# Kernel optimization log

Measured on AMD Instinct MI355X. Metric: run time of the kernel, lower is better.

The kernel has to match this reference:

```python
import jax, jax.numpy as jnp
import numpy as np

B, S, I, H = 32, 1024, 256, 256
NUM_LAYERS = 2


def _lstm_dir(x, m, h0, c0, Wih, Whh, bih, bhh, reverse=False):
    """x: [S,B,in], m: [S,B,1]. Returns outs [S,B,H], hT, cT.
    PyTorch LSTMCell gate order: i, f, g, o. Masked reset to init state per step."""
    if reverse:
        x = x[::-1]
        m = m[::-1]

    def step(carry, xm):
        h, c = carry
        xt, mt = xm
        gates = xt @ Wih.T + bih + h @ Whh.T + bhh  # [B,4H]
        i, f, g, o = jnp.split(gates, 4, axis=-1)
        i = jax.nn.sigmoid(i)
        f = jax.nn.sigmoid(f)
        g = jnp.tanh(g)
        o = jax.nn.sigmoid(o)
        cn = f * c + i * g
        hn = o * jnp.tanh(cn)
        hn = hn * mt + h0 * (1.0 - mt)
        cn = cn * mt + c0 * (1.0 - mt)
        return (hn, cn), hn

    (hT, cT), outs = jax.lax.scan(step, (h0, c0), (x, m))
    if reverse:
        outs = outs[::-1]
    return outs, hT, cT


def setup_inputs() -> dict:
    key = jax.random.key(0)
    ks = iter(jax.random.split(key, 40))
    d = {
        "inputs": jax.random.normal(next(ks), (B, S, I), dtype=jnp.float32),
        "mask": jnp.ones((B, S), dtype=jnp.float32),
    }
    scale = 0.05
    for li in range(NUM_LAYERS):
        in_sz = I if li == 0 else 2 * H
        for d_tag in ("f", "b"):
            p = f"l{li}{d_tag}_"
            d[p + "Wih"] = jax.random.normal(next(ks), (4 * H, in_sz), dtype=jnp.float32) * scale
            d[p + "Whh"] = jax.random.normal(next(ks), (4 * H, H), dtype=jnp.float32) * scale
            d[p + "bih"] = jnp.zeros((4 * H,), dtype=jnp.float32)
            d[p + "bhh"] = jnp.zeros((4 * H,), dtype=jnp.float32)
    return d


def reference(inputs, mask,
              l0f_Wih, l0f_Whh, l0f_bih, l0f_bhh,
              l0b_Wih, l0b_Whh, l0b_bih, l0b_bhh,
              l1f_Wih, l1f_Whh, l1f_bih, l1f_bhh,
              l1b_Wih, l1b_Whh, l1b_bih, l1b_bhh):
    # batch_first -> time-major
    x = jnp.transpose(inputs, (1, 0, 2))          # [S,B,I]
    m = jnp.transpose(mask, (1, 0))[:, :, None]   # [S,B,1] broadcasts over H
    h0 = jnp.zeros((B, H), dtype=inputs.dtype)
    c0 = h0

    layers = [
        ((l0f_Wih, l0f_Whh, l0f_bih, l0f_bhh), (l0b_Wih, l0b_Whh, l0b_bih, l0b_bhh)),
        ((l1f_Wih, l1f_Whh, l1f_bih, l1f_bhh), (l1b_Wih, l1b_Whh, l1b_bih, l1b_bhh)),
    ]
    hn, cn = [], []
    for fw_p, bw_p in layers:
        # (dropout between layers only active in training mode; eval reference skips it)
        fw_out, fh, fc = _lstm_dir(x, m, h0, c0, *fw_p, reverse=False)
        bw_out, bh, bc = _lstm_dir(x, m, h0, c0, *bw_p, reverse=True)
        x = jnp.concatenate((fw_out, bw_out), axis=2)  # [S,B,2H]
        hn.append(jnp.concatenate((fh, bh), axis=1))
        cn.append(jnp.concatenate((fc, bc), axis=1))

    output = jnp.transpose(x, (1, 0, 2))  # [B,S,2H]
    return output, jnp.stack(hn, axis=0), jnp.stack(cn, axis=0)
```

## Files before the change

### kernel.cpp

```cpp
#include <hip/hip_runtime.h>
#include <cstddef>

typedef __attribute__((ext_vector_type(8))) short short8;
typedef __attribute__((ext_vector_type(4))) short short4v;
typedef __attribute__((ext_vector_type(4))) float f32x4;

__device__ __forceinline__ unsigned short f2bf(float f){
  unsigned u = __builtin_bit_cast(unsigned, f);
  u += 0x7FFFu + ((u >> 16) & 1u);
  return (unsigned short)(u >> 16);
}
__device__ __forceinline__ float bf2f(unsigned short h){
  unsigned u = ((unsigned)h) << 16;
  return __builtin_bit_cast(float, u);
}
__device__ __forceinline__ float sigf(float x){
  return __builtin_amdgcn_rcpf(1.0f + __builtin_amdgcn_exp2f(-1.4426950408889634f * x));
}
__device__ __forceinline__ float tanhf_(float x){
  return 1.0f - 2.0f * __builtin_amdgcn_rcpf(1.0f + __builtin_amdgcn_exp2f(2.8853900817779268f * x));
}

__global__ __launch_bounds__(64) void cast_x(const float* __restrict__ in, unsigned short* __restrict__ xb){
  int blk = blockIdx.x;
  int t = blk & 1023, b = blk >> 10;
  int k = threadIdx.x * 4;
  float4 v = *(const float4*)(in + (size_t)blk * 256 + k);
  unsigned lo = f2bf(v.x) | ((unsigned)f2bf(v.y) << 16);
  unsigned hi = f2bf(v.z) | ((unsigned)f2bf(v.w) << 16);
  *(uint2*)(xb + ((size_t)t * 32 + b) * 256 + k) = make_uint2(lo, hi);
}

__global__ __launch_bounds__(64) void cast_w(const float* __restrict__ Wf, const float* __restrict__ Wb,
    const float* __restrict__ bihf, const float* __restrict__ bhhf,
    const float* __restrict__ bihb, const float* __restrict__ bhhb,
    unsigned short* __restrict__ Bw, float* __restrict__ bias, int K){
  int row = blockIdx.x;
  int dd = row >> 10, gc = row & 1023;
  const float* src = (dd ? Wb : Wf) + (size_t)gc * K;
  unsigned short* dst = Bw + (size_t)row * K;
  for (int k = threadIdx.x * 4; k < K; k += 256){
    float4 v = *(const float4*)(src + k);
    unsigned lo = f2bf(v.x) | ((unsigned)f2bf(v.y) << 16);
    unsigned hi = f2bf(v.z) | ((unsigned)f2bf(v.w) << 16);
    *(uint2*)(dst + k) = make_uint2(lo, hi);
  }
  if (threadIdx.x == 0)
    bias[row] = dd ? (bihb[gc] + bhhb[gc]) : (bihf[gc] + bhhf[gc]);
}

__global__ __launch_bounds__(256) void gemm_xg(const unsigned short* __restrict__ A,
    const unsigned short* __restrict__ Bw, const float* __restrict__ bias,
    unsigned short* __restrict__ xg, int K){
  __shared__ __align__(16) unsigned short Al[128 * 64];
  __shared__ __align__(16) unsigned short Bl[128 * 64];
  const int tid = threadIdx.x;
  const int w = tid >> 6, l = tid & 63, q = l >> 4, cl = l & 15;
  const int bm = blockIdx.x >> 4, bn = blockIdx.x & 15;
  const int wm = w & 1, wn = w >> 1;
  f32x4 acc[4][4];
#pragma unroll
  for (int nt = 0; nt < 4; ++nt){
    float bv = bias[bn * 128 + wn * 64 + nt * 16 + cl];
#pragma unroll
    for (int mt = 0; mt < 4; ++mt) acc[mt][nt] = (f32x4){bv, bv, bv, bv};
  }
  const unsigned short* Ab = A + (size_t)(bm * 128) * K;
  const unsigned short* Bb = Bw + (size_t)(bn * 128) * K;
  for (int k0 = 0; k0 < K; k0 += 64){
#pragma unroll
    for (int i = 0; i < 4; ++i){
      int task = tid + i * 256;
      int row = task >> 3, ch = task & 7;
      int sw = ((ch ^ (row & 7)) * 8);
      *(uint4*)(&Al[row * 64 + sw]) = *(const uint4*)(Ab + (size_t)row * K + k0 + ch * 8);
      *(uint4*)(&Bl[row * 64 + sw]) = *(const uint4*)(Bb + (size_t)row * K + k0 + ch * 8);
    }
    __syncthreads();
#pragma unroll
    for (int kt2 = 0; kt2 < 2; ++kt2){
      short8 af[4], bfv[4];
#pragma unroll
      for (int mt = 0; mt < 4; ++mt){
        int row = wm * 64 + mt * 16 + cl;
        af[mt] = *(const short8*)(&Al[row * 64 + (((kt2 * 4 + q) ^ (row & 7)) * 8)]);
      }
#pragma unroll
      for (int nt = 0; nt < 4; ++nt){
        int n = wn * 64 + nt * 16 + cl;
        bfv[nt] = *(const short8*)(&Bl[n * 64 + (((kt2 * 4 + q) ^ (n & 7)) * 8)]);
      }
#pragma unroll
      for (int mt = 0; mt < 4; ++mt)
#pragma unroll
        for (int nt = 0; nt < 4; ++nt)
          acc[mt][nt] = __builtin_amdgcn_mfma_f32_16x16x32_bf16(af[mt], bfv[nt], acc[mt][nt], 0, 0, 0);
    }
    __syncthreads();
  }
#pragma unroll
  for (int mt = 0; mt < 4; ++mt){
    int row = bm * 128 + wm * 64 + mt * 16 + q * 4;
    int tt = row >> 5, bb = row & 31;
#pragma unroll
    for (int nt = 0; nt < 4; ++nt){
      int col = bn * 128 + wn * 64 + nt * 16 + cl;
      f32x4 v = acc[mt][nt];
      unsigned lo = f2bf(v[0]) | ((unsigned)f2bf(v[1]) << 16);
      unsigned hi = f2bf(v[2]) | ((unsigned)f2bf(v[3]) << 16);
      *(uint2*)(xg + ((size_t)tt * 2048 + col) * 32 + bb) = make_uint2(lo, hi);
    }
  }
}

#define POLL1(EXTRA) \
  asm volatile("global_load_dwordx4 %0, %1, off sc1" EXTRA \
    : "=v"(pv) : "v"(pb) : "memory")

#define CHK() ( \
  xx = (pv.x ^ tagv) | (pv.y ^ tagv) | (pv.z ^ tagv) | (pv.w ^ tagv), \
  __all((xx & 0xFFFFu) == 0u) )

__global__ __launch_bounds__(512, 1) void lstm_rec(const unsigned short* __restrict__ xg,
    const float* __restrict__ WhhF, const float* __restrict__ WhhB,
    const float* __restrict__ mask, unsigned* __restrict__ hx,
    unsigned short* __restrict__ houts, float* __restrict__ out,
    float* __restrict__ hnout, float* __restrict__ cnout, int layer){
  __shared__ __align__(16) unsigned short hloc[2][16][136];
  __shared__ __align__(16) unsigned short hrem[2][16][136];
  __shared__ __align__(16) float maskL[16384];
  const int tid = threadIdx.x;
  const int w = tid >> 6, l = tid & 63, q = l >> 4, cl = l & 15;
  const int bid = blockIdx.x;
  const int ch = bid & 1, d = (bid >> 1) & 1, g = bid >> 2;
  const float* __restrict__ Whh = d ? WhhB : WhhF;
  const int jj = ch * 128 + w * 16 + cl;
  const int ph = ch ^ 1;
  const int ch4 = ch * 4, ph4 = ph * 4;

  short8 bfrag[4][8];
#pragma unroll
  for (int gi = 0; gi < 4; ++gi){
    const float* wg = Whh + (size_t)(gi * 256 + jj) * 256 + q * 8;
#pragma unroll
    for (int p = 0; p < 8; ++p){
      int gk = (p < 4) ? (ch4 + p) : (ph4 + (p - 4));
      float4 x0 = *(const float4*)(wg + gk * 32);
      float4 x1 = *(const float4*)(wg + gk * 32 + 4);
      short8 f;
      f[0] = (short)f2bf(x0.x); f[1] = (short)f2bf(x0.y); f[2] = (short)f2bf(x0.z); f[3] = (short)f2bf(x0.w);
      f[4] = (short)f2bf(x1.x); f[5] = (short)f2bf(x1.y); f[6] = (short)f2bf(x1.z); f[7] = (short)f2bf(x1.w);
      bfrag[gi][p] = f;
    }
  }
  for (int i = tid; i < 16384; i += 512){
    int tt = i >> 4, r = i & 15;
    maskL[i] = mask[(size_t)(g * 16 + r) * 1024 + tt];
  }
  __syncthreads();

  float cst[4] = {0.f, 0.f, 0.f, 0.f};
  unsigned* hxu = hx + (size_t)(d * 2 + g) * 8192;
  const int rr = 2 * w + (l >> 5);
  const int cc = l & 31;
  const unsigned* plA = hxu + rr * 256 + ph * 128 + cc * 4;
  const unsigned* plB = plA + 4096;
  unsigned* stA = hxu + (q * 4) * 256 + jj;
  unsigned* stB = stA + 4096;
  const int bq = g * 16 + q * 4;
  const size_t dj = (size_t)d * 256 + jj;
  unsigned short* hob = houts + (size_t)bq * 512 + dj;
  float* outb = out + (size_t)bq * 524288 + dj;

  const ptrdiff_t tstep = d ? -65536 : 65536;
  const unsigned short* xcur = xg + (size_t)(d ? 1023 : 0) * 65536
                               + ((size_t)d * 1024 + jj) * 32 + g * 16 + q * 4;
  short4v xp[4], xn[4];
#pragma unroll
  for (int gi = 0; gi < 4; ++gi) xp[gi] = *(const short4v*)(xcur + gi * 8192);

#pragma unroll 2
  for (int t = 0; t < 1024; ++t){
    const int par = t & 1;
    const int ot = d ? (1023 - t) : t;
    f32x4 acc[4];
    if (t > 0){
      const unsigned* pb = par ? plA : plB;
      uint4 pv;
      POLL1("");
#pragma unroll
      for (int gi = 0; gi < 4; ++gi)
        acc[gi] = (f32x4){bf2f((unsigned short)xp[gi][0]), bf2f((unsigned short)xp[gi][1]),
                          bf2f((unsigned short)xp[gi][2]), bf2f((unsigned short)xp[gi][3])};
      asm volatile("s_waitcnt vmcnt(0)" ::: "memory");
      __builtin_amdgcn_sched_barrier(0);
      const unsigned tagv = (unsigned)t;
      unsigned xx;
      if (!CHK()){
        do{
          POLL1("\n\ts_waitcnt vmcnt(0)");
          __builtin_amdgcn_sched_barrier(0);
        } while (!CHK());
      }
      if (t < 1023){
#pragma unroll
        for (int gi = 0; gi < 4; ++gi) xn[gi] = *(const short4v*)(xcur + tstep + gi * 8192);
      }
      {
        unsigned lo = __builtin_amdgcn_perm(pv.y, pv.x, 0x07060302u);
        unsigned hi = __builtin_amdgcn_perm(pv.w, pv.z, 0x07060302u);
        *(uint2*)(&hrem[par][rr][cc * 4]) = make_uint2(lo, hi);
      }
      __syncthreads();
      const unsigned short* lb = &hloc[par ^ 1][0][0];
      const unsigned short* rb = &hrem[par][0][0];
      const int ao = cl * 136 + q * 8;
#pragma unroll
      for (int ktl = 0; ktl < 4; ++ktl){
        short8 a = *(const short8*)(lb + ao + ktl * 32);
        acc[0] = __builtin_amdgcn_mfma_f32_16x16x32_bf16(a, bfrag[0][ktl], acc[0], 0, 0, 0);
        acc[1] = __builtin_amdgcn_mfma_f32_16x16x32_bf16(a, bfrag[1][ktl], acc[1], 0, 0, 0);
        acc[2] = __builtin_amdgcn_mfma_f32_16x16x32_bf16(a, bfrag[2][ktl], acc[2], 0, 0, 0);
        acc[3] = __builtin_amdgcn_mfma_f32_16x16x32_bf16(a, bfrag[3][ktl], acc[3], 0, 0, 0);
      }
#pragma unroll
      for (int ktl = 0; ktl < 4; ++ktl){
        short8 a = *(const short8*)(rb + ao + ktl * 32);
        acc[0] = __builtin_amdgcn_mfma_f32_16x16x32_bf16(a, bfrag[0][4 + ktl], acc[0], 0, 0, 0);
        acc[1] = __builtin_amdgcn_mfma_f32_16x16x32_bf16(a, bfrag[1][4 + ktl], acc[1], 0, 0, 0);
        acc[2] = __builtin_amdgcn_mfma_f32_16x16x32_bf16(a, bfrag[2][4 + ktl], acc[2], 0, 0, 0);
        acc[3] = __builtin_amdgcn_mfma_f32_16x16x32_bf16(a, bfrag[3][4 + ktl], acc[3], 0, 0, 0);
      }
    } else {
#pragma unroll
      for (int gi = 0; gi < 4; ++gi)
        acc[gi] = (f32x4){bf2f((unsigned short)xp[gi][0]), bf2f((unsigned short)xp[gi][1]),
                          bf2f((unsigned short)xp[gi][2]), bf2f((unsigned short)xp[gi][3])};
#pragma unroll
      for (int gi = 0; gi < 4; ++gi) xn[gi] = *(const short4v*)(xcur + tstep + gi * 8192);
    }
    f32x4 mv = *(const f32x4*)(&maskL[ot * 16 + q * 4]);
    float hv[4]; unsigned short hb[4];
#pragma unroll
    for (int r = 0; r < 4; ++r){
      float ig = sigf(acc[0][r]);
      float fg = sigf(acc[1][r]);
      float gg = tanhf_(acc[2][r]);
      float og = sigf(acc[3][r]);
      float cn = fg * cst[r] + ig * gg;
      float hn = og * tanhf_(cn);
      float m = mv[r];
      hn *= m; cn *= m;
      cst[r] = cn; hv[r] = hn; hb[r] = f2bf(hn);
    }
    unsigned* sw = par ? stB : stA;
    const unsigned tagn = (unsigned)(t + 1);
#pragma unroll
    for (int r = 0; r < 4; ++r)
      __hip_atomic_store(sw + r * 256, ((unsigned)hb[r] << 16) | tagn,
                         __ATOMIC_RELAXED, __HIP_MEMORY_SCOPE_AGENT);
#pragma unroll
    for (int r = 0; r < 4; ++r) hloc[par][q * 4 + r][w * 16 + cl] = hb[r];
    if (layer == 0){
#pragma unroll
      for (int r = 0; r < 4; ++r) hob[(size_t)ot * 16384 + r * 512] = hb[r];
    } else {
#pragma unroll
      for (int r = 0; r < 4; ++r) outb[(size_t)r * 524288 + (size_t)ot * 512] = hv[r];
    }
    if (t == 1023){
#pragma unroll
      for (int r = 0; r < 4; ++r){
        size_t bo = (size_t)(layer * 32 + bq + r) * 512 + dj;
        hnout[bo] = hv[r];
        cnout[bo] = cst[r];
      }
    }
    if (t < 1023){
#pragma unroll
      for (int gi = 0; gi < 4; ++gi) xp[gi] = xn[gi];
    }
    xcur += tstep;
  }
}

extern "C" void kernel_launch(void* const* d_in, const int* in_sizes, int n_in,
                              void* d_out, int out_size, void* d_ws, size_t ws_size,
                              hipStream_t stream){
  const float* inputs  = (const float*)d_in[0];
  const float* mask    = (const float*)d_in[1];
  const float* l0f_Wih = (const float*)d_in[2];
  const float* l0f_Whh = (const float*)d_in[3];
  const float* l0f_bih = (const float*)d_in[4];
  const float* l0f_bhh = (const float*)d_in[5];
  const float* l0b_Wih = (const float*)d_in[6];
  const float* l0b_Whh = (const float*)d_in[7];
  const float* l0b_bih = (const float*)d_in[8];
  const float* l0b_bhh = (const float*)d_in[9];
  const float* l1f_Wih = (const float*)d_in[10];
  const float* l1f_Whh = (const float*)d_in[11];
  const float* l1f_bih = (const float*)d_in[12];
  const float* l1f_bhh = (const float*)d_in[13];
  const float* l1b_Wih = (const float*)d_in[14];
  const float* l1b_Whh = (const float*)d_in[15];
  const float* l1b_bih = (const float*)d_in[16];
  const float* l1b_bhh = (const float*)d_in[17];

  char* ws = (char*)d_ws;
  unsigned short* xg   = (unsigned short*)(ws);
  unsigned short* xbf  = (unsigned short*)(ws + 134217728);
  unsigned short* hout = (unsigned short*)(ws + 150994944);
  unsigned short* B0   = (unsigned short*)(ws + 184549376);
  unsigned short* B1   = (unsigned short*)(ws + 185597952);
  float* bias0         = (float*)(ws + 187695104);
  float* bias1         = (float*)(ws + 187703296);
  unsigned* hx         = (unsigned*)(ws + 187711488);

  float* out   = (float*)d_out;
  float* hnout = out + 16777216;
  float* cnout = hnout + 32768;

  hipMemsetAsync(hx, 0, 262144, stream);
  cast_x<<<32768, 64, 0, stream>>>(inputs, xbf);
  cast_w<<<2048, 64, 0, stream>>>(l0f_Wih, l0b_Wih, l0f_bih, l0f_bhh, l0b_bih, l0b_bhh, B0, bias0, 256);
  cast_w<<<2048, 64, 0, stream>>>(l1f_Wih, l1b_Wih, l1f_bih, l1f_bhh, l1b_bih, l1b_bhh, B1, bias1, 512);
  gemm_xg<<<4096, 256, 0, stream>>>(xbf, B0, bias0, xg, 256);
  lstm_rec<<<8, 512, 0, stream>>>(xg, l0f_Whh, l0b_Whh, mask, hx, hout, nullptr, hnout, cnout, 0);
  gemm_xg<<<4096, 256, 0, stream>>>(hout, B1, bias1, xg, 512);
  lstm_rec<<<8, 512, 0, stream>>>(xg, l1f_Whh, l1b_Whh, mask, hx + 32768, nullptr, out, hnout, cnout, 1);
}
```

Baseline: 4.525 ms.

## Rework cross-block handoff: dual-cache polling, dual stores, XCD-aware block placement

Launches 16 blocks and keeps 8, picking the partner blocks so that the two halves of each direction/batch pair are 8 block IDs apart. Under round-robin XCD dispatch this likely places them on the same XCD, or at least changes their placement. Each poll now issues two loads at different cache scopes (sc0 and sc1), and each h exchange is stored twice at the matching scopes, so the partner can see the data through a nearer cache. The __syncthreads is replaced with an explicit lgkmcnt wait plus s_barrier, and the xg prefetch moves outside the poll path. This adds extra memory traffic and relies on assumptions about dispatch order and cache coherence.

```diff
diff --git a/kernel.cpp b/kernel.cpp
--- a/kernel.cpp
+++ b/kernel.cpp
@@ -113,12 +113,18 @@
   }
 }
 
-#define POLL1(EXTRA) \
-  asm volatile("global_load_dwordx4 %0, %1, off sc1" EXTRA \
-    : "=v"(pv) : "v"(pb) : "memory")
-
-#define CHK() ( \
-  xx = (pv.x ^ tagv) | (pv.y ^ tagv) | (pv.z ^ tagv) | (pv.w ^ tagv), \
+#define ISSUE2() \
+  asm volatile("global_load_dwordx4 %0, %2, off sc0\n\t" \
+               "global_load_dwordx4 %1, %2, off sc1" \
+    : "=v"(pvF), "=v"(pvS) : "v"(pb) : "memory")
+#define WAITF() \
+  asm volatile("s_waitcnt vmcnt(1)" ::: "memory"); \
+  __builtin_amdgcn_sched_barrier(0)
+#define WAITS() \
+  asm volatile("s_waitcnt vmcnt(0)" ::: "memory"); \
+  __builtin_amdgcn_sched_barrier(0)
+#define CHKV(P) ( \
+  xx = (P.x ^ tagv) | (P.y ^ tagv) | (P.z ^ tagv) | (P.w ^ tagv), \
   __all((xx & 0xFFFFu) == 0u) )
 
 __global__ __launch_bounds__(512, 1) void lstm_rec(const unsigned short* __restrict__ xg,
@@ -132,7 +138,9 @@
   const int tid = threadIdx.x;
   const int w = tid >> 6, l = tid & 63, q = l >> 4, cl = l & 15;
   const int bid = blockIdx.x;
-  const int ch = bid & 1, d = (bid >> 1) & 1, g = bid >> 2;
+  const int pair = bid & 7, ch = bid >> 3;
+  if (pair >= 4) return;
+  const int d = pair >> 1, g = pair & 1;
   const float* __restrict__ Whh = d ? WhhB : WhhF;
   const int jj = ch * 128 + w * 16 + cl;
   const int ph = ch ^ 1;
@@ -184,34 +192,37 @@
     const int par = t & 1;
     const int ot = d ? (1023 - t) : t;
     f32x4 acc[4];
+#pragma unroll
+    for (int gi = 0; gi < 4; ++gi)
+      acc[gi] = (f32x4){bf2f((unsigned short)xp[gi][0]), bf2f((unsigned short)xp[gi][1]),
+                        bf2f((unsigned short)xp[gi][2]), bf2f((unsigned short)xp[gi][3])};
+    __builtin_amdgcn_sched_barrier(0);
     if (t > 0){
       const unsigned* pb = par ? plA : plB;
-      uint4 pv;
-      POLL1("");
-#pragma unroll
-      for (int gi = 0; gi < 4; ++gi)
-        acc[gi] = (f32x4){bf2f((unsigned short)xp[gi][0]), bf2f((unsigned short)xp[gi][1]),
-                          bf2f((unsigned short)xp[gi][2]), bf2f((unsigned short)xp[gi][3])};
-      asm volatile("s_waitcnt vmcnt(0)" ::: "memory");
-      __builtin_amdgcn_sched_barrier(0);
+      uint4 pvF, pvS;
+      ISSUE2();
+      WAITF();
       const unsigned tagv = (unsigned)t;
-      unsigned xx;
-      if (!CHK()){
-        do{
-          POLL1("\n\ts_waitcnt vmcnt(0)");
-          __builtin_amdgcn_sched_barrier(0);
-        } while (!CHK());
-      }
-      if (t < 1023){
-#pragma unroll
-        for (int gi = 0; gi < 4; ++gi) xn[gi] = *(const short4v*)(xcur + tstep + gi * 8192);
+      unsigned xx; uint4 pv;
+      if (CHKV(pvF)) pv = pvF;
+      else {
+        for (;;){
+          WAITS();
+          if (CHKV(pvS)) { pv = pvS; break; }
+          ISSUE2();
+          WAITF();
+          if (CHKV(pvF)) { pv = pvF; break; }
+        }
       }
       {
         unsigned lo = __builtin_amdgcn_perm(pv.y, pv.x, 0x07060302u);
         unsigned hi = __builtin_amdgcn_perm(pv.w, pv.z, 0x07060302u);
         *(uint2*)(&hrem[par][rr][cc * 4]) = make_uint2(lo, hi);
       }
-      __syncthreads();
+      asm volatile("s_waitcnt lgkmcnt(0)" ::: "memory");
+      __builtin_amdgcn_s_barrier();
+      asm volatile("" ::: "memory");
+      __builtin_amdgcn_sched_barrier(0);
       const unsigned short* lb = &hloc[par ^ 1][0][0];
       const unsigned short* rb = &hrem[par][0][0];
       const int ao = cl * 136 + q * 8;
@@ -231,11 +242,11 @@
         acc[2] = __builtin_amdgcn_mfma_f32_16x16x32_bf16(a, bfrag[2][4 + ktl], acc[2], 0, 0, 0);
         acc[3] = __builtin_amdgcn_mfma_f32_16x16x32_bf16(a, bfrag[3][4 + ktl], acc[3], 0, 0, 0);
       }
-    } else {
-#pragma unroll
-      for (int gi = 0; gi < 4; ++gi)
-        acc[gi] = (f32x4){bf2f((unsigned short)xp[gi][0]), bf2f((unsigned short)xp[gi][1]),
-                          bf2f((unsigned short)xp[gi][2]), bf2f((unsigned short)xp[gi][3])};
+      asm volatile("s_waitcnt vmcnt(0)" ::: "memory");
+      asm volatile("" :: "v"(pvS.x), "v"(pvS.y), "v"(pvS.z), "v"(pvS.w));
+      __builtin_amdgcn_sched_barrier(0);
+    }
+    if (t < 1023){
 #pragma unroll
       for (int gi = 0; gi < 4; ++gi) xn[gi] = *(const short4v*)(xcur + tstep + gi * 8192);
     }
@@ -253,12 +264,25 @@
       hn *= m; cn *= m;
       cst[r] = cn; hv[r] = hn; hb[r] = f2bf(hn);
     }
-    unsigned* sw = par ? stB : stA;
-    const unsigned tagn = (unsigned)(t + 1);
-#pragma unroll
-    for (int r = 0; r < 4; ++r)
-      __hip_atomic_store(sw + r * 256, ((unsigned)hb[r] << 16) | tagn,
-                         __ATOMIC_RELAXED, __HIP_MEMORY_SCOPE_AGENT);
+    {
+      unsigned* sw = par ? stB : stA;
+      const unsigned tagn = (unsigned)(t + 1);
+      unsigned w0 = ((unsigned)hb[0] << 16) | tagn;
+      unsigned w1 = ((unsigned)hb[1] << 16) | tagn;
+      unsigned w2 = ((unsigned)hb[2] << 16) | tagn;
+      unsigned w3 = ((unsigned)hb[3] << 16) | tagn;
+      asm volatile(
+        "global_store_dword %0, %1, off\n\t"
+        "global_store_dword %0, %2, off offset:1024\n\t"
+        "global_store_dword %0, %3, off offset:2048\n\t"
+        "global_store_dword %0, %4, off offset:3072\n\t"
+        "global_store_dword %0, %1, off sc1\n\t"
+        "global_store_dword %0, %2, off offset:1024 sc1\n\t"
+        "global_store_dword %0, %3, off offset:2048 sc1\n\t"
+        "global_store_dword %0, %4, off offset:3072 sc1"
+        :: "v"(sw), "v"(w0), "v"(w1), "v"(w2), "v"(w3)
+        : "memory");
+    }
 #pragma unroll
     for (int r = 0; r < 4; ++r) hloc[par][q * 4 + r][w * 16 + cl] = hb[r];
     if (layer == 0){
@@ -325,7 +349,7 @@
   cast_w<<<2048, 64, 0, stream>>>(l0f_Wih, l0b_Wih, l0f_bih, l0f_bhh, l0b_bih, l0b_bhh, B0, bias0, 256);
   cast_w<<<2048, 64, 0, stream>>>(l1f_Wih, l1b_Wih, l1f_bih, l1f_bhh, l1b_bih, l1b_bhh, B1, bias1, 512);
   gemm_xg<<<4096, 256, 0, stream>>>(xbf, B0, bias0, xg, 256);
-  lstm_rec<<<8, 512, 0, stream>>>(xg, l0f_Whh, l0b_Whh, mask, hx, hout, nullptr, hnout, cnout, 0);
+  lstm_rec<<<16, 512, 0, stream>>>(xg, l0f_Whh, l0b_Whh, mask, hx, hout, nullptr, hnout, cnout, 0);
   gemm_xg<<<4096, 256, 0, stream>>>(hout, B1, bias1, xg, 512);
-  lstm_rec<<<8, 512, 0, stream>>>(xg, l1f_Whh, l1b_Whh, mask, hx + 32768, nullptr, out, hnout, cnout, 1);
-}
+  lstm_rec<<<16, 512, 0, stream>>>(xg, l1f_Whh, l1b_Whh, mask, hx + 32768, nullptr, out, hnout, cnout, 1);
+}
```

Measured after the change: 7.257 ms. 1.6x slower.
